# Kernel optimization log

Measured on AMD Instinct MI355X. Metric: run time of the kernel, lower is better.

The kernel has to match this reference:

```python
import jax, jax.numpy as jnp
import numpy as np

B = 64          # batch
N = 256         # input_dim (number of MPS sites / pixels)
BOND = 128      # bond dimension
DF = 2          # feature dimension per pixel
OUT = 10        # output classes
EPS = 1e-12


def _xavier_uniform(key, shape, fan_in, fan_out, gain):
    bound = gain * np.sqrt(6.0 / (fan_in + fan_out))
    return jax.random.uniform(key, shape, jnp.float32, -bound, bound)


def setup_inputs() -> dict:
    key = jax.random.key(0)
    k_x, k_c0, k_cr, k_cl = jax.random.split(key, 4)
    gain = float(np.sqrt(2.0 / (1.0 + 0.01 ** 2)))  # leaky_relu gain
    x = jax.random.uniform(k_x, (B, N), dtype=jnp.float32)  # pixels in [0,1]
    # core 0: (1, DF, BOND); torch fan_in = DF*BOND, fan_out = 1*BOND
    core0 = _xavier_uniform(k_c0, (1, DF, BOND), DF * BOND, BOND, gain)
    # remaining N-1 cores: (BOND, DF, BOND); fan_in = DF*BOND, fan_out = BOND*BOND... torch: fan_in = shape[1]*shape[2] = DF*BOND, fan_out = shape[0]*shape[2] = BOND*BOND? No: fan_out = shape[0]*prod(shape[2:]) = BOND*BOND
    cores = _xavier_uniform(k_cr, (N - 1, BOND, DF, BOND), DF * BOND, BOND * BOND, gain)
    classifier = _xavier_uniform(k_cl, (OUT, BOND), BOND, OUT, gain)
    return {"x": x, "core0": core0, "cores": cores, "classifier": classifier}


def _mps_forward(x, core0, cores, classifier):
    b = x.shape[0]
    H = core0.shape[-1]
    # feature map: pixel v -> (1-v, v)
    feats = jnp.stack([1.0 - x, x], axis=-1)                  # (B, N, DF)
    # contract each core with its pixel feature
    special = jnp.einsum('ldh,bd->blh', core0, feats[:, 0])   # (B, 1, H)
    others = jnp.einsum('nldh,bnd->bnlh', cores, feats[:, 1:])  # (B, N-1, H, H)
    log_norm = jnp.zeros((b,), dtype=x.dtype)

    # log-depth tree contraction; loop bound is static (trace-time)
    while 1 + others.shape[1] > 1:
        # pad the special (1,H) leftmost tensor up to (H,H) with zero rows
        padded = jnp.pad(special, ((0, 0), (0, H - special.shape[1]), (0, 0)))
        full = jnp.concatenate([padded[:, None], others], axis=1)  # (B, K, H, H)
        K = full.shape[1]
        odd = (K % 2 != 0)
        if odd:
            last = full[:, -1]
            full = full[:, :-1]
        s1 = full[:, 0::2]                                    # (B, P, H, H)
        s2 = full[:, 1::2]
        cp = jnp.matmul(s1, s2)                               # (B, P, H, H)
        norms = jnp.maximum(
            jnp.sqrt(jnp.sum(cp * cp, axis=(-2, -1))), EPS)   # (B, P)
        log_norm = log_norm + jnp.sum(jnp.log(norms), axis=1)
        cp = cp / norms[:, :, None, None]
        special = cp[:, 0, 0:1, :]                            # keep only row 0
        others = cp[:, 1:]
        if odd:
            others = jnp.concatenate([others, last[:, None]], axis=1)

    mps_out = special[:, 0, :]                                # (B, H)
    logits = mps_out @ classifier.T + log_norm[:, None]      # (B, OUT)
    return logits


def reference(x, core0, cores, classifier):
    return _mps_forward(x, core0, cores, classifier)
```

## Files before the change

### kernel.cpp

```cpp
#include <hip/hip_runtime.h>
#include <stdint.h>


typedef unsigned short u16;
typedef __attribute__((ext_vector_type(8))) short short8;
typedef __attribute__((ext_vector_type(4))) float f32x4;

#define HP 136

__device__ __forceinline__ u16 f2b(float f) {
  uint32_t u = __builtin_bit_cast(uint32_t, f);
  u += 0x7FFFu + ((u >> 16) & 1u);
  return (u16)(u >> 16);
}
__device__ __forceinline__ float b2f(u16 b) {
  uint32_t u = ((uint32_t)b) << 16;
  return __builtin_bit_cast(float, u);
}

struct AccW { f32x4 t[2][2]; };

__device__ __forceinline__ void mfma_w16(const u16* Alds, const u16* Blds,
                                         AccW& acc) {
  const int tid = threadIdx.x;
  const int wid = tid >> 6, lane = tid & 63;
  const int wm = (wid >> 2) * 32, wn = (wid & 3) * 32;
  const int l16 = lane & 15, quad = lane >> 4;
#pragma unroll
  for (int tm = 0; tm < 2; tm++)
#pragma unroll
    for (int tn = 0; tn < 2; tn++)
      acc.t[tm][tn] = (f32x4){0.f, 0.f, 0.f, 0.f};
#pragma unroll
  for (int kk = 0; kk < 128; kk += 32) {
    short8 af[2], bf[2];
#pragma unroll
    for (int t = 0; t < 2; t++) {
      af[t] = *(const short8*)(Alds + (wm + t * 16 + l16) * HP + kk + quad * 8);
      bf[t] = *(const short8*)(Blds + (wn + t * 16 + l16) * HP + kk + quad * 8);
    }
#pragma unroll
    for (int tm = 0; tm < 2; tm++)
#pragma unroll
      for (int tn = 0; tn < 2; tn++)
        acc.t[tm][tn] = __builtin_amdgcn_mfma_f32_16x16x32_bf16(
            af[tm], bf[tn], acc.t[tm][tn], 0, 0, 0);
  }
}

__device__ __forceinline__ float acc_sumsq(const AccW& acc) {
  float ss = 0.f;
#pragma unroll
  for (int tm = 0; tm < 2; tm++)
#pragma unroll
    for (int tn = 0; tn < 2; tn++)
#pragma unroll
      for (int i = 0; i < 4; i++) {
        float v = acc.t[tm][tn][i];
        ss += v * v;
      }
  return ss;
}

__device__ __forceinline__ void bounce_store(u16* Lb, const AccW& acc, float scale,
                                             bool transposed) {
  const int tid = threadIdx.x;
  const int wid = tid >> 6, lane = tid & 63;
  const int wm = (wid >> 2) * 32, wn = (wid & 3) * 32;
  const int l16 = lane & 15, quad = lane >> 4;
#pragma unroll
  for (int tm = 0; tm < 2; tm++)
#pragma unroll
    for (int tn = 0; tn < 2; tn++)
#pragma unroll
      for (int i = 0; i < 4; i++) {
        int r = wm + tm * 16 + quad * 4 + i;
        int c = wn + tn * 16 + l16;
        int key = transposed ? c : r, sec = transposed ? r : c;
        Lb[key * HP + sec] = f2b(acc.t[tm][tn][i] * scale);
      }
}

__device__ __forceinline__ void copy_out(const u16* Lb, u16* out) {
  const int tid = threadIdx.x;
#pragma unroll
  for (int i = 0; i < 2; i++) {
    int g8 = tid + i * 1024;
    int row = g8 >> 4, c8 = g8 & 15;
    *(uint4*)(out + g8 * 8) = *(const uint4*)(Lb + row * HP + c8 * 8);
  }
}

__device__ __forceinline__ void loadM(u16* Lb, const u16* __restrict__ src) {
  const int tid = threadIdx.x;
#pragma unroll
  for (int i = 0; i < 2; i++) {
    int g8 = tid + i * 1024;
    int r = g8 >> 4, c8 = g8 & 15;
    *(uint4*)(Lb + r * HP + c8 * 8) = *(const uint4*)(src + g8 * 8);
  }
}

__device__ __forceinline__ float block_sum(float v, float* red, int nw) {
#pragma unroll
  for (int off = 32; off > 0; off >>= 1) v += __shfl_down(v, off);
  int wid = threadIdx.x >> 6;
  if ((threadIdx.x & 63) == 0) red[wid] = v;
  __syncthreads();
  if (threadIdx.x == 0) {
    float s = 0.f;
    for (int w = 0; w < nw; w++) s += red[w];
    red[0] = s;
  }
  __syncthreads();
  float s = red[0];
  __syncthreads();
  return s;
}

__global__ __launch_bounds__(1024) void k1(const float* __restrict__ cores,
                                           u16* __restrict__ T) {
  __shared__ u16 Ald[128 * HP], B0[128 * HP], B1[128 * HP];
  const int j = blockIdx.x;
  const int p = blockIdx.y;
  const float* c1 = cores + (size_t)(2 * j + 1) * 32768;
  const float* c2 = cores + (size_t)(2 * j + 2) * 32768;
  const int tid = threadIdx.x;
#pragma unroll 4
  for (int i = 0; i < 16; i++) {
    int lh = tid + i * 1024;
    int l = lh >> 7, h = lh & 127;
    float a0 = c1[(l * 2 + 0) * 128 + h];
    float av = p ? (c1[(l * 2 + 1) * 128 + h] - a0) : a0;
    Ald[l * HP + h] = f2b(av);
    float b0 = c2[(l * 2 + 0) * 128 + h];
    float b1 = c2[(l * 2 + 1) * 128 + h];
    B0[h * HP + l] = f2b(b0);
    B1[h * HP + l] = f2b(b1 - b0);
  }
  __syncthreads();
  const bool tr = (j % 2) == 0;
  u16* Tj = T + ((size_t)j * 4 + p * 2) * 16384;
  AccW q0, q1;
  mfma_w16(Ald, B0, q0);
  mfma_w16(Ald, B1, q1);
  __syncthreads();
  bounce_store(Ald, q0, 1.f, tr); __syncthreads();
  copy_out(Ald, Tj + 0 * 16384);  __syncthreads();
  bounce_store(Ald, q1, 1.f, tr); __syncthreads();
  copy_out(Ald, Tj + 1 * 16384);
}

__global__ __launch_bounds__(1024, 8) void k1b(const u16* __restrict__ T,
                                               u16* __restrict__ TT) {
  __shared__ u16 Ald[128 * HP], Bld[128 * HP];
  const int t = blockIdx.x;
  const int j2 = blockIdx.y;
  const int m1 = 2 * j2 + 1, m2 = 2 * j2 + 2;
  const u16* TA = T + ((size_t)m1 * 4 + (t >> 2)) * 16384;
  const u16* TB = T + ((size_t)m2 * 4 + (t & 3)) * 16384;
  loadM(Ald, TA);
  loadM(Bld, TB);
  __syncthreads();
  AccW acc;
  mfma_w16(Ald, Bld, acc);
  __syncthreads();
  bounce_store(Ald, acc, 1.f, (j2 % 2) == 0);
  __syncthreads();
  copy_out(Ald, TT + ((size_t)j2 * 16 + t) * 16384);
}

__global__ __launch_bounds__(256) void k1c(const u16* __restrict__ TT,
                                           float* __restrict__ Gpart) {
  __shared__ float Gp[1024];
  const int j2 = blockIdx.x, kc = blockIdx.y;
  const int tid = threadIdx.x;
  const int w = tid >> 6, lane = tid & 63;
  const int l16 = lane & 15, quad = lane >> 4;
  const u16* V = TT + (size_t)j2 * 16 * 16384 + (size_t)l16 * 16384;
  const int k0 = kc * 4096 + w * 1024;
  f32x4 acc = (f32x4){0.f, 0.f, 0.f, 0.f};
  for (int kk = k0; kk < k0 + 1024; kk += 32) {
    short8 av = *(const short8*)(V + kk + quad * 8);
    acc = __builtin_amdgcn_mfma_f32_16x16x32_bf16(av, av, acc, 0, 0, 0);
  }
#pragma unroll
  for (int i = 0; i < 4; i++)
    Gp[w * 256 + (quad * 4 + i) * 16 + l16] = acc[i];
  __syncthreads();
  Gpart[((size_t)j2 * 4 + kc) * 256 + tid] =
      Gp[tid] + Gp[256 + tid] + Gp[512 + tid] + Gp[768 + tid];
}

__global__ __launch_bounds__(128) void k2ns(const float* __restrict__ x,
                                            const float* __restrict__ Gpart,
                                            const float* __restrict__ core0,
                                            const float* __restrict__ cores,
                                            const u16* __restrict__ T,
                                            float* __restrict__ cbuf,
                                            float* __restrict__ sA,
                                            float* __restrict__ logs) {
  __shared__ float Gs[256];
  __shared__ float svec[128];
  __shared__ float red[8];
  const int bx = blockIdx.x, tid = threadIdx.x;
  if (bx < 63) {
    const int j2 = bx;
#pragma unroll
    for (int i = 0; i < 2; i++) {
      int t2 = tid + i * 128;
      float s = 0.f;
#pragma unroll
      for (int kc = 0; kc < 4; kc++)
        s += Gpart[((size_t)j2 * 4 + kc) * 256 + t2];
      Gs[t2] = s;
    }
    __syncthreads();
    if (tid < 64) {
      const int b = tid;
      const float* xb = x + b * 256;
      const int m1 = 2 * j2 + 1, m2 = 2 * j2 + 2;
      float a1 = xb[2 * m1 + 2], b1 = xb[2 * m1 + 3];
      float a2 = xb[2 * m2 + 2], b2 = xb[2 * m2 + 3];
      float c1[4] = {1.f, b1, a1, a1 * b1};
      float c2[4] = {1.f, b2, a2, a2 * b2};
      float c[16];
#pragma unroll
      for (int p = 0; p < 4; p++)
#pragma unroll
        for (int q = 0; q < 4; q++) c[p * 4 + q] = c1[p] * c2[q];
      float n2 = 0.f;
#pragma unroll
      for (int t = 0; t < 16; t++) {
        float s = 0.f;
#pragma unroll
        for (int u = 0; u < 16; u++) s += Gs[t * 16 + u] * c[u];
        n2 += c[t] * s;
      }
      float n = fmaxf(sqrtf(n2), 1e-12f);
      logs[b * 127 + 1 + j2] = logf(n);
      float inv = 1.f / n;
#pragma unroll
      for (int t = 0; t < 16; t++)
        cbuf[((size_t)j2 * 64 + b) * 16 + t] = c[t] * inv;
    }
  } else {
    const int b = bx - 63;
    const float* xb = x + b * 256;
    float x0 = xb[0], x1 = xb[1];
    svec[tid] = core0[tid] * (1.f - x0) + core0[128 + tid] * x0;
    __syncthreads();
    float acc1 = 0.f;
    for (int k = 0; k < 128; k++) {
      float m0 = cores[(k * 2 + 0) * 128 + tid];
      float m1 = cores[(k * 2 + 1) * 128 + tid];
      acc1 += svec[k] * (m0 + x1 * (m1 - m0));
    }
    float tot = block_sum(acc1 * acc1, red, 2);
    float n1 = fmaxf(sqrtf(tot), 1e-12f);
    float ln = logf(n1);
    svec[tid] = acc1 / n1;
    __syncthreads();
    float a = xb[2], bb = xb[3], ab = a * bb;
    float acc2 = 0.f;
    for (int k8 = 0; k8 < 16; k8++) {
      union { uint4 v; u16 s[8]; } q00, q01, q10, q11;
      q00.v = *(const uint4*)(T + tid * 128 + k8 * 8);
      q01.v = *(const uint4*)(T + 16384 + tid * 128 + k8 * 8);
      q10.v = *(const uint4*)(T + 32768 + tid * 128 + k8 * 8);
      q11.v = *(const uint4*)(T + 49152 + tid * 128 + k8 * 8);
#pragma unroll
      for (int e = 0; e < 8; e++) {
        float pk = b2f(q00.s[e]) + a * b2f(q10.s[e]) + bb * b2f(q01.s[e]) +
                   ab * b2f(q11.s[e]);
        acc2 += svec[k8 * 8 + e] * pk;
      }
    }
    float tot2 = block_sum(acc2 * acc2, red, 2);
    float n2 = fmaxf(sqrtf(tot2), 1e-12f);
    sA[b * 128 + tid] = acc2 / n2;
    if (tid == 0) logs[b * 127 + 0] = ln + logf(n2);
  }
}

__global__ __launch_bounds__(256, 4) void k2c(const u16* __restrict__ TT,
                                              const float* __restrict__ cbuf,
                                              u16* __restrict__ M0) {
  const int slice = blockIdx.x;
  const int j2 = blockIdx.y;
  const int tid = threadIdx.x;
  const int e0 = slice * 1024 + tid * 4;
  float v[16][4];
#pragma unroll
  for (int t = 0; t < 16; t++) {
    union { uint2 u; u16 s[4]; } q;
    q.u = *(const uint2*)(TT + ((size_t)j2 * 16 + t) * 16384 + e0);
#pragma unroll
    for (int e = 0; e < 4; e++) v[t][e] = b2f(q.s[e]);
  }
  const float4* cb4 = (const float4*)(cbuf + (size_t)j2 * 1024);
  u16* out = M0 + (size_t)j2 * 16384 + e0;
#pragma unroll 4
  for (int b = 0; b < 64; b++) {
    float4 c0 = cb4[b * 4 + 0];
    float4 c1 = cb4[b * 4 + 1];
    float4 c2 = cb4[b * 4 + 2];
    float4 c3 = cb4[b * 4 + 3];
    float cc[16] = {c0.x, c0.y, c0.z, c0.w, c1.x, c1.y, c1.z, c1.w,
                    c2.x, c2.y, c2.z, c2.w, c3.x, c3.y, c3.z, c3.w};
    float o[4] = {0.f, 0.f, 0.f, 0.f};
#pragma unroll
    for (int t = 0; t < 16; t++)
#pragma unroll
      for (int e = 0; e < 4; e++) o[e] += cc[t] * v[t][e];
    union { uint2 u; u16 s[4]; } r;
#pragma unroll
    for (int e = 0; e < 4; e++) r.s[e] = f2b(o[e]);
    *(uint2*)(out + (size_t)b * 63 * 16384) = r.u;
  }
}

__global__ __launch_bounds__(1024, 4) void round2x(const u16* __restrict__ In,
                                                   u16* __restrict__ Out,
                                                   const float* __restrict__ sIn,
                                                   float* __restrict__ sOut,
                                                   float* __restrict__ logs,
                                                   int count_in, int count_out,
                                                   int slot0, int slot1) {
  __shared__ u16 L0[128 * HP], L1[128 * HP], L2[128 * HP], L3[128 * HP];
  __shared__ float red[16];
  const int b = blockIdx.y, p = blockIdx.x, tid = threadIdx.x;
  const u16* base = In + (size_t)b * count_in * 16384;
  if (p == 0) {
    float* svf = (float*)L3;
    float* svf2 = svf + 128;
    if (tid < 128) svf[tid] = sIn[b * 128 + tid];
    loadM(L0, base + 1 * 16384);
    loadM(L1, base + 2 * 16384);
    __syncthreads();
    float acc0 = 0.f;
    if (tid < 128) {
      for (int k8 = 0; k8 < 16; k8++) {
        union { uint4 v; u16 s[8]; } q;
        q.v = *(const uint4*)(base + tid * 128 + k8 * 8);
#pragma unroll
        for (int e = 0; e < 8; e++) acc0 += svf[k8 * 8 + e] * b2f(q.s[e]);
      }
    }
    float t0 = block_sum((tid < 128) ? acc0 * acc0 : 0.f, red, 16);
    float n0 = fmaxf(sqrtf(t0), 1e-12f);
    if (tid == 0) logs[b * 127 + slot0] = logf(n0);
    if (tid < 128) svf2[tid] = acc0 / n0;
    AccW acc;
    mfma_w16(L0, L1, acc);
    float tq = block_sum(acc_sumsq(acc), red, 16);
    float nq = fmaxf(sqrtf(tq), 1e-12f);
    if (tid == 0) logs[b * 127 + slot0 + 1] = logf(nq);
    bounce_store(L2, acc, 1.f / nq, true);
    __syncthreads();
    float acc2 = 0.f;
    if (tid < 128) {
      for (int l = 0; l < 128; l++) acc2 += svf2[l] * b2f(L2[tid * HP + l]);
    }
    float t2 = block_sum((tid < 128) ? acc2 * acc2 : 0.f, red, 16);
    float n2 = fmaxf(sqrtf(t2), 1e-12f);
    if (tid == 0) logs[b * 127 + slot1] = logf(n2);
    if (tid < 128) sOut[b * 128 + tid] = acc2 / n2;
  } else {
    const int m = p - 1;
    loadM(L0, base + (size_t)(4 * m + 3) * 16384);
    loadM(L1, base + (size_t)(4 * m + 4) * 16384);
    __syncthreads();
    loadM(L2, base + (size_t)(4 * m + 5) * 16384);
    loadM(L3, base + (size_t)(4 * m + 6) * 16384);
    AccW acc;
    mfma_w16(L0, L1, acc);
    float t1 = block_sum(acc_sumsq(acc), red, 16);
    float n1 = fmaxf(sqrtf(t1), 1e-12f);
    if (tid == 0) logs[b * 127 + slot0 + 2 + 2 * m] = logf(n1);
    bounce_store(L0, acc, 1.f / n1, false);
    mfma_w16(L2, L3, acc);
    float t2 = block_sum(acc_sumsq(acc), red, 16);
    float n2 = fmaxf(sqrtf(t2), 1e-12f);
    if (tid == 0) logs[b * 127 + slot0 + 3 + 2 * m] = logf(n2);
    bounce_store(L1, acc, 1.f / n2, true);
    __syncthreads();
    mfma_w16(L0, L1, acc);
    float t3 = block_sum(acc_sumsq(acc), red, 16);
    float n3 = fmaxf(sqrtf(t3), 1e-12f);
    if (tid == 0) logs[b * 127 + slot1 + 1 + m] = logf(n3);
    bounce_store(L2, acc, 1.f / n3, (m % 2) == 0);
    __syncthreads();
    copy_out(L2, Out + ((size_t)b * count_out + m) * 16384);
  }
}

__global__ __launch_bounds__(1024, 8) void r7f(const u16* __restrict__ In,
                                               const float* __restrict__ sIn,
                                               const float* __restrict__ logs,
                                               const float* __restrict__ cls,
                                               float* __restrict__ out) {
  __shared__ u16 Ald[128 * HP], Bld[128 * HP];
  __shared__ float svec[128], ovec[128], red[16];
  const int b = blockIdx.x, tid = threadIdx.x;
  if (tid < 128) svec[tid] = sIn[b * 128 + tid];
  const u16* A = In + ((size_t)b * 3 + 1) * 16384;
  const u16* Bm = In + ((size_t)b * 3 + 2) * 16384;
  loadM(Ald, A);
  loadM(Bld, Bm);
  __syncthreads();
  AccW acc;
  mfma_w16(Ald, Bld, acc);
  float tot = block_sum(acc_sumsq(acc), red, 16);
  float n1 = fmaxf(sqrtf(tot), 1e-12f);
  float lg = logf(n1);
  bounce_store(Ald, acc, 1.f / n1, true);
  const u16* M0p = In + (size_t)b * 3 * 16384;
  float acc0 = 0.f;
  if (tid < 128) {
    for (int k8 = 0; k8 < 16; k8++) {
      union { uint4 v; u16 s[8]; } q;
      q.v = *(const uint4*)(M0p + tid * 128 + k8 * 8);
#pragma unroll
      for (int e = 0; e < 8; e++) acc0 += svec[k8 * 8 + e] * b2f(q.s[e]);
    }
  }
  float tot0 = block_sum((tid < 128) ? acc0 * acc0 : 0.f, red, 16);
  float n0 = fmaxf(sqrtf(tot0), 1e-12f);
  lg += logf(n0);
  if (tid < 128) ovec[tid] = acc0 / n0;
  __syncthreads();
  float acc2 = 0.f;
  if (tid < 128) {
    for (int r = 0; r < 128; r++) acc2 += ovec[r] * b2f(Ald[tid * HP + r]);
  }
  float tot2 = block_sum((tid < 128) ? acc2 * acc2 : 0.f, red, 16);
  float n2 = fmaxf(sqrtf(tot2), 1e-12f);
  lg += logf(n2);
  if (tid < 128) svec[tid] = acc2 / n2;
  __syncthreads();
  if (tid < 10) {
    float a = 0.f;
    for (int h = 0; h < 128; h++) a += svec[h] * cls[tid * 128 + h];
    float L = lg;
    for (int i = 0; i < 124; i++) L += logs[b * 127 + i];
    out[b * 10 + tid] = a + L;
  }
}

extern "C" void kernel_launch(void* const* d_in, const int* in_sizes, int n_in,
                              void* d_out, int out_size, void* d_ws, size_t ws_size,
                              hipStream_t stream) {
  (void)in_sizes; (void)n_in; (void)out_size; (void)ws_size;
  const float* x     = (const float*)d_in[0];
  const float* core0 = (const float*)d_in[1];
  const float* cores = (const float*)d_in[2];
  const float* cls   = (const float*)d_in[3];
  float* out = (float*)d_out;
  char* ws = (char*)d_ws;

  constexpr size_t SZ_T  = (size_t)127 * 4 * 16384 * 2;
  constexpr size_t SZ_A  = (size_t)64 * 31 * 16384 * 2;
  constexpr size_t SZ_M0 = (size_t)64 * 63 * 16384 * 2;

  u16*   T    = (u16*)(ws);
  u16*   TT   = (u16*)(ws + SZ_T);
  u16*   M2   = (u16*)(ws);
  u16*   M0   = (u16*)(ws + SZ_A);
  char*  tail0 = ws + SZ_A + SZ_M0;
  float* Gpart = (float*)(tail0);
  float* cbuf = (float*)(tail0 + 262144);
  float* sA   = (float*)(tail0 + 262144 + 262144);
  float* sB   = (float*)(tail0 + 262144 + 262144 + 32768);
  float* logs = (float*)(tail0 + 262144 + 262144 + 65536);

  k1  <<<dim3(127, 2), 1024, 0, stream>>>(cores, T);
  k1b <<<dim3(16, 63), 1024, 0, stream>>>(T, TT);
  k1c <<<dim3(63, 4), 256, 0, stream>>>(TT, Gpart);
  k2ns<<<dim3(127), 128, 0, stream>>>(x, Gpart, core0, cores, T, cbuf, sA, logs);
  k2c <<<dim3(16, 63), 256, 0, stream>>>(TT, cbuf, M0);
  round2x<<<dim3(16, 64), 1024, 0, stream>>>(M0, M2, sA, sB, logs, 63, 15, 64, 96);
  round2x<<<dim3(4, 64), 1024, 0, stream>>>(M2, M0, sB, sA, logs, 15, 3, 112, 120);
  r7f  <<<dim3(64), 1024, 0, stream>>>(M0, sA, logs, cls, out);
}
```

Baseline: 255.0 us.

## Persistent round-2 kernel with register prefetch of next task's four matrices

Replaces the first round2x launch (16x64 blocks, one task each) with round2xp, which runs 4x64 blocks that each loop over up to four tasks. While the current task's MFMA products run, the four input matrices for the next task are prefetched into registers and then written to LDS, hiding global load latency. It also adds a cheaper 16-wave block reduction that needs fewer barriers. The cost is fewer blocks in flight (less parallelism), higher register pressure from the prefetch buffers, and a serial chain of tasks inside each block.

```diff
diff --git a/kernel.cpp b/kernel.cpp
--- a/kernel.cpp
+++ b/kernel.cpp
@@ -115,6 +115,17 @@
   __syncthreads();
   float s = red[0];
   __syncthreads();
+  return s;
+}
+
+__device__ __forceinline__ float bsum16(float v, float* red) {
+#pragma unroll
+  for (int off = 32; off > 0; off >>= 1) v += __shfl_down(v, off);
+  if ((threadIdx.x & 63) == 0) red[threadIdx.x >> 6] = v;
+  __syncthreads();
+  float s = 0.f;
+#pragma unroll
+  for (int w = 0; w < 16; w++) s += red[w];
   return s;
 }
 
@@ -317,6 +328,140 @@
 #pragma unroll
     for (int e = 0; e < 4; e++) r.s[e] = f2b(o[e]);
     *(uint2*)(out + (size_t)b * 63 * 16384) = r.u;
+  }
+}
+
+struct Pref { uint4 r[4][2]; };
+
+__device__ __forceinline__ void pref_load4(Pref& P, const u16* base, int i0,
+                                           int i1, int i2, int i3) {
+  const int tid = threadIdx.x;
+  const u16* s0 = base + (size_t)i0 * 16384;
+  const u16* s1 = base + (size_t)i1 * 16384;
+  const u16* s2 = base + (size_t)i2 * 16384;
+  const u16* s3 = base + (size_t)i3 * 16384;
+#pragma unroll
+  for (int i = 0; i < 2; i++) {
+    int g8 = (tid + i * 1024) * 8;
+    P.r[0][i] = *(const uint4*)(s0 + g8);
+    P.r[1][i] = *(const uint4*)(s1 + g8);
+    P.r[2][i] = *(const uint4*)(s2 + g8);
+    P.r[3][i] = *(const uint4*)(s3 + g8);
+  }
+}
+
+__device__ __forceinline__ void pref_store(const Pref& P, u16* L0, u16* L1,
+                                           u16* L2, u16* L3) {
+  u16* Ls[4] = {L0, L1, L2, L3};
+  const int tid = threadIdx.x;
+#pragma unroll
+  for (int q = 0; q < 4; q++)
+#pragma unroll
+    for (int i = 0; i < 2; i++) {
+      int g8 = tid + i * 1024;
+      *(uint4*)(Ls[q] + (g8 >> 4) * HP + (g8 & 15) * 8) = P.r[q][i];
+    }
+}
+
+__device__ __forceinline__ void task_idx(int bx, int k, int npair, int& i0,
+                                         int& i1, int& i2, int& i3) {
+  if (k < npair) {
+    int m = bx + 4 * k;
+    i0 = 4 * m + 3; i1 = 4 * m + 4; i2 = 4 * m + 5; i3 = 4 * m + 6;
+  } else {
+    i0 = 1; i1 = 2; i2 = 1; i3 = 2;
+  }
+}
+
+__global__ __launch_bounds__(1024, 4) void round2xp(const u16* __restrict__ In,
+                                                    u16* __restrict__ Out,
+                                                    const float* __restrict__ sIn,
+                                                    float* __restrict__ sOut,
+                                                    float* __restrict__ logs) {
+  __shared__ u16 L0[128 * HP], L1[128 * HP], L2[128 * HP], L3[128 * HP];
+  __shared__ __align__(16) float red[48];
+  const int b = blockIdx.y, bx = blockIdx.x, tid = threadIdx.x;
+  const u16* base = In + (size_t)b * 63 * 16384;
+  const int npair = (bx < 3) ? 4 : 3;
+  const int ntask = 4;
+
+  Pref P;
+  {
+    int a0, a1, a2, a3;
+    task_idx(bx, 0, npair, a0, a1, a2, a3);
+    pref_load4(P, base, a0, a1, a2, a3);
+    pref_store(P, L0, L1, L2, L3);
+    task_idx(bx, 1, npair, a0, a1, a2, a3);
+    pref_load4(P, base, a0, a1, a2, a3);
+  }
+  __syncthreads();
+
+  for (int k = 0; k < ntask; k++) {
+    if (k < npair) {
+      const int m = bx + 4 * k;
+      AccW acc;
+      mfma_w16(L0, L1, acc);
+      float t1 = bsum16(acc_sumsq(acc), red);
+      float n1 = fmaxf(sqrtf(t1), 1e-12f);
+      if (tid == 0) logs[b * 127 + 66 + 2 * m] = logf(n1);
+      bounce_store(L0, acc, 1.f / n1, false);
+      mfma_w16(L2, L3, acc);
+      float t2 = bsum16(acc_sumsq(acc), red + 16);
+      float n2 = fmaxf(sqrtf(t2), 1e-12f);
+      if (tid == 0) logs[b * 127 + 67 + 2 * m] = logf(n2);
+      bounce_store(L1, acc, 1.f / n2, true);
+      __syncthreads();
+      mfma_w16(L0, L1, acc);
+      float t3 = bsum16(acc_sumsq(acc), red + 32);
+      float n3 = fmaxf(sqrtf(t3), 1e-12f);
+      if (tid == 0) logs[b * 127 + 97 + m] = logf(n3);
+      bounce_store(L2, acc, 1.f / n3, (m % 2) == 0);
+      __syncthreads();
+      copy_out(L2, Out + ((size_t)b * 15 + m) * 16384);
+    } else {
+      float* svf = (float*)L3;
+      float* svf2 = svf + 128;
+      if (tid < 128) svf[tid] = sIn[b * 128 + tid];
+      __syncthreads();
+      float acc0 = 0.f;
+      if (tid < 128) {
+        for (int k8 = 0; k8 < 16; k8++) {
+          union { uint4 v; u16 s[8]; } q;
+          q.v = *(const uint4*)(base + tid * 128 + k8 * 8);
+#pragma unroll
+          for (int e = 0; e < 8; e++) acc0 += svf[k8 * 8 + e] * b2f(q.s[e]);
+        }
+      }
+      float t0 = bsum16((tid < 128) ? acc0 * acc0 : 0.f, red);
+      float n0 = fmaxf(sqrtf(t0), 1e-12f);
+      if (tid == 0) logs[b * 127 + 64] = logf(n0);
+      if (tid < 128) svf2[tid] = acc0 / n0;
+      AccW acc;
+      mfma_w16(L0, L1, acc);
+      float tq = bsum16(acc_sumsq(acc), red + 16);
+      float nq = fmaxf(sqrtf(tq), 1e-12f);
+      if (tid == 0) logs[b * 127 + 65] = logf(nq);
+      bounce_store(L2, acc, 1.f / nq, true);
+      __syncthreads();
+      float acc2 = 0.f;
+      if (tid < 128) {
+        for (int l = 0; l < 128; l++) acc2 += svf2[l] * b2f(L2[tid * HP + l]);
+      }
+      float t2 = bsum16((tid < 128) ? acc2 * acc2 : 0.f, red + 32);
+      float n2 = fmaxf(sqrtf(t2), 1e-12f);
+      if (tid == 0) logs[b * 127 + 96] = logf(n2);
+      if (tid < 128) sOut[b * 128 + tid] = acc2 / n2;
+    }
+    if (k + 1 < ntask) {
+      __syncthreads();
+      pref_store(P, L0, L1, L2, L3);
+      if (k + 2 < ntask) {
+        int a0, a1, a2, a3;
+        task_idx(bx, k + 2, npair, a0, a1, a2, a3);
+        pref_load4(P, base, a0, a1, a2, a3);
+      }
+      __syncthreads();
+    }
   }
 }
 
@@ -479,7 +624,7 @@
   k1c <<<dim3(63, 4), 256, 0, stream>>>(TT, Gpart);
   k2ns<<<dim3(127), 128, 0, stream>>>(x, Gpart, core0, cores, T, cbuf, sA, logs);
   k2c <<<dim3(16, 63), 256, 0, stream>>>(TT, cbuf, M0);
-  round2x<<<dim3(16, 64), 1024, 0, stream>>>(M0, M2, sA, sB, logs, 63, 15, 64, 96);
-  round2x<<<dim3(4, 64), 1024, 0, stream>>>(M2, M0, sB, sA, logs, 15, 3, 112, 120);
+  round2xp<<<dim3(4, 64), 1024, 0, stream>>>(M0, M2, sA, sB, logs);
+  round2x <<<dim3(4, 64), 1024, 0, stream>>>(M2, M0, sB, sA, logs, 15, 3, 112, 120);
   r7f  <<<dim3(64), 1024, 0, stream>>>(M0, sA, logs, cls, out);
 }
```

Result: slower. 293.9 us (+15.2%).

## Feed MFMA fragments directly from global memory and merge block reductions

Applied to the files above, without the earlier changes.

Adds a matmul helper that loads MFMA operand fragments straight from global memory instead of first staging the whole matrix in LDS. k1b and round2x use it, which removes the staging copies and barriers and cuts LDS use in round2x from four tiles to three, possibly allowing more resident blocks. The block reductions are restructured: two norms are reduced together, and a lighter reduction has every thread sum the per-wave partials, which saves barriers. Each global element is now read by four waves rather than once, so the change relies on L2/L1 caching and accepts less coalesced access.

```diff
diff --git a/kernel.cpp b/kernel.cpp
--- a/kernel.cpp
+++ b/kernel.cpp
@@ -38,6 +38,35 @@
     for (int t = 0; t < 2; t++) {
       af[t] = *(const short8*)(Alds + (wm + t * 16 + l16) * HP + kk + quad * 8);
       bf[t] = *(const short8*)(Blds + (wn + t * 16 + l16) * HP + kk + quad * 8);
+    }
+#pragma unroll
+    for (int tm = 0; tm < 2; tm++)
+#pragma unroll
+      for (int tn = 0; tn < 2; tn++)
+        acc.t[tm][tn] = __builtin_amdgcn_mfma_f32_16x16x32_bf16(
+            af[tm], bf[tn], acc.t[tm][tn], 0, 0, 0);
+  }
+}
+
+__device__ __forceinline__ void mfma_w16_g(const u16* __restrict__ Ag,
+                                           const u16* __restrict__ Bg,
+                                           AccW& acc) {
+  const int tid = threadIdx.x;
+  const int wid = tid >> 6, lane = tid & 63;
+  const int wm = (wid >> 2) * 32, wn = (wid & 3) * 32;
+  const int l16 = lane & 15, quad = lane >> 4;
+#pragma unroll
+  for (int tm = 0; tm < 2; tm++)
+#pragma unroll
+    for (int tn = 0; tn < 2; tn++)
+      acc.t[tm][tn] = (f32x4){0.f, 0.f, 0.f, 0.f};
+#pragma unroll
+  for (int kk = 0; kk < 128; kk += 32) {
+    short8 af[2], bf[2];
+#pragma unroll
+    for (int t = 0; t < 2; t++) {
+      af[t] = *(const short8*)(Ag + (size_t)(wm + t * 16 + l16) * 128 + kk + quad * 8);
+      bf[t] = *(const short8*)(Bg + (size_t)(wn + t * 16 + l16) * 128 + kk + quad * 8);
     }
 #pragma unroll
     for (int tm = 0; tm < 2; tm++)
@@ -91,16 +120,6 @@
   }
 }
 
-__device__ __forceinline__ void loadM(u16* Lb, const u16* __restrict__ src) {
-  const int tid = threadIdx.x;
-#pragma unroll
-  for (int i = 0; i < 2; i++) {
-    int g8 = tid + i * 1024;
-    int r = g8 >> 4, c8 = g8 & 15;
-    *(uint4*)(Lb + r * HP + c8 * 8) = *(const uint4*)(src + g8 * 8);
-  }
-}
-
 __device__ __forceinline__ float block_sum(float v, float* red, int nw) {
 #pragma unroll
   for (int off = 32; off > 0; off >>= 1) v += __shfl_down(v, off);
@@ -116,6 +135,39 @@
   float s = red[0];
   __syncthreads();
   return s;
+}
+
+__device__ __forceinline__ float bsum16(float v, float* red) {
+#pragma unroll
+  for (int off = 32; off > 0; off >>= 1) v += __shfl_down(v, off);
+  if ((threadIdx.x & 63) == 0) red[threadIdx.x >> 6] = v;
+  __syncthreads();
+  float s = 0.f;
+#pragma unroll
+  for (int w = 0; w < 16; w++) s += red[w];
+  return s;
+}
+
+__device__ __forceinline__ void bsum16x2(float v1, float v2, float* red,
+                                         float& o1, float& o2) {
+#pragma unroll
+  for (int off = 32; off > 0; off >>= 1) {
+    v1 += __shfl_down(v1, off);
+    v2 += __shfl_down(v2, off);
+  }
+  if ((threadIdx.x & 63) == 0) {
+    red[threadIdx.x >> 6] = v1;
+    red[16 + (threadIdx.x >> 6)] = v2;
+  }
+  __syncthreads();
+  float s1 = 0.f, s2 = 0.f;
+#pragma unroll
+  for (int w = 0; w < 16; w++) {
+    s1 += red[w];
+    s2 += red[16 + w];
+  }
+  o1 = s1;
+  o2 = s2;
 }
 
 __global__ __launch_bounds__(1024) void k1(const float* __restrict__ cores,
@@ -153,18 +205,14 @@
 
 __global__ __launch_bounds__(1024, 8) void k1b(const u16* __restrict__ T,
                                                u16* __restrict__ TT) {
-  __shared__ u16 Ald[128 * HP], Bld[128 * HP];
+  __shared__ u16 Ald[128 * HP];
   const int t = blockIdx.x;
   const int j2 = blockIdx.y;
   const int m1 = 2 * j2 + 1, m2 = 2 * j2 + 2;
   const u16* TA = T + ((size_t)m1 * 4 + (t >> 2)) * 16384;
   const u16* TB = T + ((size_t)m2 * 4 + (t & 3)) * 16384;
-  loadM(Ald, TA);
-  loadM(Bld, TB);
-  __syncthreads();
   AccW acc;
-  mfma_w16(Ald, Bld, acc);
-  __syncthreads();
+  mfma_w16_g(TA, TB, acc);
   bounce_store(Ald, acc, 1.f, (j2 % 2) == 0);
   __syncthreads();
   copy_out(Ald, TT + ((size_t)j2 * 16 + t) * 16384);
@@ -327,16 +375,15 @@
                                                    float* __restrict__ logs,
                                                    int count_in, int count_out,
                                                    int slot0, int slot1) {
-  __shared__ u16 L0[128 * HP], L1[128 * HP], L2[128 * HP], L3[128 * HP];
-  __shared__ float red[16];
+  __shared__ u16 L0[128 * HP], L1[128 * HP], L2[128 * HP];
+  __shared__ float svf[256];
+  __shared__ float red[32];
   const int b = blockIdx.y, p = blockIdx.x, tid = threadIdx.x;
   const u16* base = In + (size_t)b * count_in * 16384;
   if (p == 0) {
-    float* svf = (float*)L3;
-    float* svf2 = svf + 128;
     if (tid < 128) svf[tid] = sIn[b * 128 + tid];
-    loadM(L0, base + 1 * 16384);
-    loadM(L1, base + 2 * 16384);
+    AccW accq;
+    mfma_w16_g(base + 1 * 16384, base + 2 * 16384, accq);
     __syncthreads();
     float acc0 = 0.f;
     if (tid < 128) {
@@ -347,49 +394,49 @@
         for (int e = 0; e < 8; e++) acc0 += svf[k8 * 8 + e] * b2f(q.s[e]);
       }
     }
-    float t0 = block_sum((tid < 128) ? acc0 * acc0 : 0.f, red, 16);
+    float t0, tq;
+    bsum16x2((tid < 128) ? acc0 * acc0 : 0.f, acc_sumsq(accq), red, t0, tq);
     float n0 = fmaxf(sqrtf(t0), 1e-12f);
-    if (tid == 0) logs[b * 127 + slot0] = logf(n0);
-    if (tid < 128) svf2[tid] = acc0 / n0;
-    AccW acc;
-    mfma_w16(L0, L1, acc);
-    float tq = block_sum(acc_sumsq(acc), red, 16);
     float nq = fmaxf(sqrtf(tq), 1e-12f);
-    if (tid == 0) logs[b * 127 + slot0 + 1] = logf(nq);
-    bounce_store(L2, acc, 1.f / nq, true);
+    if (tid == 0) {
+      logs[b * 127 + slot0] = logf(n0);
+      logs[b * 127 + slot0 + 1] = logf(nq);
+    }
+    if (tid < 128) svf[128 + tid] = acc0 / n0;
+    bounce_store(L0, accq, 1.f / nq, true);
     __syncthreads();
     float acc2 = 0.f;
     if (tid < 128) {
-      for (int l = 0; l < 128; l++) acc2 += svf2[l] * b2f(L2[tid * HP + l]);
-    }
-    float t2 = block_sum((tid < 128) ? acc2 * acc2 : 0.f, red, 16);
+      for (int l = 0; l < 128; l++) acc2 += svf[128 + l] * b2f(L0[tid * HP + l]);
+    }
+    float t2 = bsum16((tid < 128) ? acc2 * acc2 : 0.f, red);
     float n2 = fmaxf(sqrtf(t2), 1e-12f);
     if (tid == 0) logs[b * 127 + slot1] = logf(n2);
     if (tid < 128) sOut[b * 128 + tid] = acc2 / n2;
   } else {
     const int m = p - 1;
-    loadM(L0, base + (size_t)(4 * m + 3) * 16384);
-    loadM(L1, base + (size_t)(4 * m + 4) * 16384);
-    __syncthreads();
-    loadM(L2, base + (size_t)(4 * m + 5) * 16384);
-    loadM(L3, base + (size_t)(4 * m + 6) * 16384);
-    AccW acc;
-    mfma_w16(L0, L1, acc);
-    float t1 = block_sum(acc_sumsq(acc), red, 16);
+    AccW a1, a2;
+    mfma_w16_g(base + (size_t)(4 * m + 3) * 16384,
+               base + (size_t)(4 * m + 4) * 16384, a1);
+    mfma_w16_g(base + (size_t)(4 * m + 5) * 16384,
+               base + (size_t)(4 * m + 6) * 16384, a2);
+    float t1, t2;
+    bsum16x2(acc_sumsq(a1), acc_sumsq(a2), red, t1, t2);
     float n1 = fmaxf(sqrtf(t1), 1e-12f);
-    if (tid == 0) logs[b * 127 + slot0 + 2 + 2 * m] = logf(n1);
-    bounce_store(L0, acc, 1.f / n1, false);
-    mfma_w16(L2, L3, acc);
-    float t2 = block_sum(acc_sumsq(acc), red, 16);
     float n2 = fmaxf(sqrtf(t2), 1e-12f);
-    if (tid == 0) logs[b * 127 + slot0 + 3 + 2 * m] = logf(n2);
-    bounce_store(L1, acc, 1.f / n2, true);
-    __syncthreads();
-    mfma_w16(L0, L1, acc);
-    float t3 = block_sum(acc_sumsq(acc), red, 16);
+    if (tid == 0) {
+      logs[b * 127 + slot0 + 2 + 2 * m] = logf(n1);
+      logs[b * 127 + slot0 + 3 + 2 * m] = logf(n2);
+    }
+    bounce_store(L0, a1, 1.f / n1, false);
+    bounce_store(L1, a2, 1.f / n2, true);
+    __syncthreads();
+    AccW a3;
+    mfma_w16(L0, L1, a3);
+    float t3 = bsum16(acc_sumsq(a3), red);
     float n3 = fmaxf(sqrtf(t3), 1e-12f);
     if (tid == 0) logs[b * 127 + slot1 + 1 + m] = logf(n3);
-    bounce_store(L2, acc, 1.f / n3, (m % 2) == 0);
+    bounce_store(L2, a3, 1.f / n3, (m % 2) == 0);
     __syncthreads();
     copy_out(L2, Out + ((size_t)b * count_out + m) * 16384);
   }
@@ -406,8 +453,13 @@
   if (tid < 128) svec[tid] = sIn[b * 128 + tid];
   const u16* A = In + ((size_t)b * 3 + 1) * 16384;
   const u16* Bm = In + ((size_t)b * 3 + 2) * 16384;
-  loadM(Ald, A);
-  loadM(Bld, Bm);
+#pragma unroll
+  for (int i = 0; i < 2; i++) {
+    int g8 = tid + i * 1024;
+    int r = g8 >> 4, c8 = g8 & 15;
+    *(uint4*)(Ald + r * HP + c8 * 8) = *(const uint4*)(A + g8 * 8);
+    *(uint4*)(Bld + r * HP + c8 * 8) = *(const uint4*)(Bm + g8 * 8);
+  }
   __syncthreads();
   AccW acc;
   mfma_w16(Ald, Bld, acc);
```

Result: slower. 317.9 us (+24.7%).

## Defer intermediate norm rescaling and halve LDS buffers in tree rounds

Applied to the files above, without the earlier changes.

Drops the per-product Frobenius-norm reductions on intermediate products in round2x and r7f. Those products are stored unscaled, their log slots are written as zero, and only the final product of each group is normalized. This relies on the overall result being scale-invariant, with the log terms absorbing the scale. Round2x now reuses two LDS matrix buffers instead of four, which allows more resident blocks, at the cost of serializing the second pair of loads behind the first MFMA. A lighter 16-wave sum that needs only one barrier replaces some block_sum calls. The risk is reduced dynamic-range headroom, since intermediates are no longer rescaled.

```diff
diff --git a/kernel.cpp b/kernel.cpp
--- a/kernel.cpp
+++ b/kernel.cpp
@@ -115,6 +115,17 @@
   __syncthreads();
   float s = red[0];
   __syncthreads();
+  return s;
+}
+
+__device__ __forceinline__ float bsum16(float v, float* red) {
+#pragma unroll
+  for (int off = 32; off > 0; off >>= 1) v += __shfl_down(v, off);
+  if ((threadIdx.x & 63) == 0) red[threadIdx.x >> 6] = v;
+  __syncthreads();
+  float s = 0.f;
+#pragma unroll
+  for (int w = 0; w < 16; w++) s += red[w];
   return s;
 }
 
@@ -327,13 +338,12 @@
                                                    float* __restrict__ logs,
                                                    int count_in, int count_out,
                                                    int slot0, int slot1) {
-  __shared__ u16 L0[128 * HP], L1[128 * HP], L2[128 * HP], L3[128 * HP];
+  __shared__ u16 L0[128 * HP], L1[128 * HP];
+  __shared__ float svf[256];
   __shared__ float red[16];
   const int b = blockIdx.y, p = blockIdx.x, tid = threadIdx.x;
   const u16* base = In + (size_t)b * count_in * 16384;
   if (p == 0) {
-    float* svf = (float*)L3;
-    float* svf2 = svf + 128;
     if (tid < 128) svf[tid] = sIn[b * 128 + tid];
     loadM(L0, base + 1 * 16384);
     loadM(L1, base + 2 * 16384);
@@ -347,22 +357,21 @@
         for (int e = 0; e < 8; e++) acc0 += svf[k8 * 8 + e] * b2f(q.s[e]);
       }
     }
-    float t0 = block_sum((tid < 128) ? acc0 * acc0 : 0.f, red, 16);
-    float n0 = fmaxf(sqrtf(t0), 1e-12f);
-    if (tid == 0) logs[b * 127 + slot0] = logf(n0);
-    if (tid < 128) svf2[tid] = acc0 / n0;
-    AccW acc;
-    mfma_w16(L0, L1, acc);
-    float tq = block_sum(acc_sumsq(acc), red, 16);
-    float nq = fmaxf(sqrtf(tq), 1e-12f);
-    if (tid == 0) logs[b * 127 + slot0 + 1] = logf(nq);
-    bounce_store(L2, acc, 1.f / nq, true);
+    AccW accq;
+    mfma_w16(L0, L1, accq);
+    __syncthreads();
+    bounce_store(L0, accq, 1.f, true);
+    if (tid < 128) svf[128 + tid] = acc0;
+    if (tid == 0) {
+      logs[b * 127 + slot0] = 0.f;
+      logs[b * 127 + slot0 + 1] = 0.f;
+    }
     __syncthreads();
     float acc2 = 0.f;
     if (tid < 128) {
-      for (int l = 0; l < 128; l++) acc2 += svf2[l] * b2f(L2[tid * HP + l]);
-    }
-    float t2 = block_sum((tid < 128) ? acc2 * acc2 : 0.f, red, 16);
+      for (int l = 0; l < 128; l++) acc2 += svf[128 + l] * b2f(L0[tid * HP + l]);
+    }
+    float t2 = bsum16((tid < 128) ? acc2 * acc2 : 0.f, red);
     float n2 = fmaxf(sqrtf(t2), 1e-12f);
     if (tid == 0) logs[b * 127 + slot1] = logf(n2);
     if (tid < 128) sOut[b * 128 + tid] = acc2 / n2;
@@ -371,27 +380,30 @@
     loadM(L0, base + (size_t)(4 * m + 3) * 16384);
     loadM(L1, base + (size_t)(4 * m + 4) * 16384);
     __syncthreads();
-    loadM(L2, base + (size_t)(4 * m + 5) * 16384);
-    loadM(L3, base + (size_t)(4 * m + 6) * 16384);
-    AccW acc;
-    mfma_w16(L0, L1, acc);
-    float t1 = block_sum(acc_sumsq(acc), red, 16);
-    float n1 = fmaxf(sqrtf(t1), 1e-12f);
-    if (tid == 0) logs[b * 127 + slot0 + 2 + 2 * m] = logf(n1);
-    bounce_store(L0, acc, 1.f / n1, false);
-    mfma_w16(L2, L3, acc);
-    float t2 = block_sum(acc_sumsq(acc), red, 16);
-    float n2 = fmaxf(sqrtf(t2), 1e-12f);
-    if (tid == 0) logs[b * 127 + slot0 + 3 + 2 * m] = logf(n2);
-    bounce_store(L1, acc, 1.f / n2, true);
-    __syncthreads();
-    mfma_w16(L0, L1, acc);
-    float t3 = block_sum(acc_sumsq(acc), red, 16);
+    AccW a1;
+    mfma_w16(L0, L1, a1);
+    __syncthreads();
+    loadM(L0, base + (size_t)(4 * m + 5) * 16384);
+    loadM(L1, base + (size_t)(4 * m + 6) * 16384);
+    __syncthreads();
+    AccW a2;
+    mfma_w16(L0, L1, a2);
+    __syncthreads();
+    bounce_store(L0, a1, 1.f, false);
+    bounce_store(L1, a2, 1.f, true);
+    if (tid == 0) {
+      logs[b * 127 + slot0 + 2 + 2 * m] = 0.f;
+      logs[b * 127 + slot0 + 3 + 2 * m] = 0.f;
+    }
+    __syncthreads();
+    AccW a3;
+    mfma_w16(L0, L1, a3);
+    float t3 = bsum16(acc_sumsq(a3), red);
     float n3 = fmaxf(sqrtf(t3), 1e-12f);
     if (tid == 0) logs[b * 127 + slot1 + 1 + m] = logf(n3);
-    bounce_store(L2, acc, 1.f / n3, (m % 2) == 0);
-    __syncthreads();
-    copy_out(L2, Out + ((size_t)b * count_out + m) * 16384);
+    bounce_store(L0, a3, 1.f / n3, (m % 2) == 0);
+    __syncthreads();
+    copy_out(L0, Out + ((size_t)b * count_out + m) * 16384);
   }
 }
 
@@ -404,17 +416,11 @@
   __shared__ float svec[128], ovec[128], red[16];
   const int b = blockIdx.x, tid = threadIdx.x;
   if (tid < 128) svec[tid] = sIn[b * 128 + tid];
-  const u16* A = In + ((size_t)b * 3 + 1) * 16384;
-  const u16* Bm = In + ((size_t)b * 3 + 2) * 16384;
-  loadM(Ald, A);
-  loadM(Bld, Bm);
+  loadM(Ald, In + ((size_t)b * 3 + 1) * 16384);
+  loadM(Bld, In + ((size_t)b * 3 + 2) * 16384);
   __syncthreads();
   AccW acc;
   mfma_w16(Ald, Bld, acc);
-  float tot = block_sum(acc_sumsq(acc), red, 16);
-  float n1 = fmaxf(sqrtf(tot), 1e-12f);
-  float lg = logf(n1);
-  bounce_store(Ald, acc, 1.f / n1, true);
   const u16* M0p = In + (size_t)b * 3 * 16384;
   float acc0 = 0.f;
   if (tid < 128) {
@@ -425,19 +431,18 @@
       for (int e = 0; e < 8; e++) acc0 += svec[k8 * 8 + e] * b2f(q.s[e]);
     }
   }
-  float tot0 = block_sum((tid < 128) ? acc0 * acc0 : 0.f, red, 16);
-  float n0 = fmaxf(sqrtf(tot0), 1e-12f);
-  lg += logf(n0);
-  if (tid < 128) ovec[tid] = acc0 / n0;
+  __syncthreads();
+  bounce_store(Ald, acc, 1.f, true);
+  if (tid < 128) ovec[tid] = acc0;
   __syncthreads();
   float acc2 = 0.f;
   if (tid < 128) {
     for (int r = 0; r < 128; r++) acc2 += ovec[r] * b2f(Ald[tid * HP + r]);
   }
-  float tot2 = block_sum((tid < 128) ? acc2 * acc2 : 0.f, red, 16);
-  float n2 = fmaxf(sqrtf(tot2), 1e-12f);
-  lg += logf(n2);
-  if (tid < 128) svec[tid] = acc2 / n2;
+  float tot = bsum16((tid < 128) ? acc2 * acc2 : 0.f, red);
+  float n = fmaxf(sqrtf(tot), 1e-12f);
+  float lg = logf(n);
+  if (tid < 128) svec[tid] = acc2 / n;
   __syncthreads();
   if (tid < 10) {
     float a = 0.f;
```

Measured after the change: 247.3 us. 3.0% less time.
